# Kernel optimization log

Hardware: AMD Instinct MI355X
Metric: run time of the kernel (lower is better)

Reference implementation:

```python
import jax, jax.numpy as jnp
import numpy as np
import math

K_HEADS = 16  # nb_heads from init_kwargs


def setup_inputs() -> dict:
    key = jax.random.key(0)
    ks = jax.random.split(key, 7)
    B, M, H, D = 2, 2048, 1024, 1024 // K_HEADS
    return {
        "h": jax.random.normal(ks[0], (B, M, H), jnp.float32),
        "h_cache": jax.random.normal(ks[1], (B, M, H), jnp.float32),
        "key_pe": jax.random.normal(ks[2], (1, D, M), jnp.float32),
        "Wq": jax.random.normal(ks[3], (H, H), jnp.float32) * 0.02,
        "Wk": jax.random.normal(ks[4], (H, H), jnp.float32) * 0.02,
        "Wv": jax.random.normal(ks[5], (H, H), jnp.float32) * 0.02,
        "Wo": jax.random.normal(ks[6], (H, H), jnp.float32) * 0.02,
    }


def _heads(x, K):
    # [B, M, H] -> [B, K, M, D]
    B, M, H = x.shape
    return x.reshape(B, M, K, H // K).transpose(0, 2, 1, 3)


def reference(h, h_cache, key_pe, Wq, Wk, Wv, Wo):
    B, M, H = h.shape
    K = K_HEADS
    D = H // K
    q = _heads(h @ Wq.T, K)        # [B, K, M, D]
    k = _heads(h_cache @ Wk.T, K)  # [B, K, L, D], L == M
    v = _heads(h_cache @ Wv.T, K)  # [B, K, L, D]

    attn_cont = jnp.einsum("bkmd,bkld->bkml", q, k)            # content scores
    attn_pos = jnp.einsum("bkmd,dl->bkml", q, key_pe[0])       # positional scores
    attn = (attn_cont + attn_pos[..., :M]) / math.sqrt(D)
    attn = jax.nn.softmax(attn, axis=-1)  # computed as in source, but source
    # (faithfully) multiplies VALUE by attn_cont, not attn:
    out = jnp.einsum("bkml,bkld->bkmd", attn_cont, v)          # [B, K, M, D]
    out = out.transpose(0, 2, 1, 3).reshape(B, M, H)
    return out @ Wo.T
```

## Files before the change

kernel.cpp:

```cpp
#include <hip/hip_runtime.h>
#include <hip/hip_bf16.h>

#define BB 2
#define MM 2048
#define HH 1024
#define KH 16

typedef short s16x8 __attribute__((ext_vector_type(8)));
typedef float f32x4 __attribute__((ext_vector_type(4)));
typedef float f32x16 __attribute__((ext_vector_type(16)));

#define GLOBAL_AS __attribute__((address_space(1)))
#define LDS_AS    __attribute__((address_space(3)))

__device__ __forceinline__ void async_copy16(const void* g, void* l) {
    __builtin_amdgcn_global_load_lds((const GLOBAL_AS void*)g, (LDS_AS void*)l, 16, 0, 0);
}

struct __align__(8) bf16x4_t { __hip_bfloat16 x, y, z, w; };

__global__ __launch_bounds__(256) void cvt_all(
    const float* __restrict__ h_f, const float* __restrict__ hc_f,
    const float* __restrict__ Wk_f, const float* __restrict__ Wv_f,
    const float* __restrict__ Wo_f, const float* __restrict__ Wq_f,
    __hip_bfloat16* __restrict__ hb, __hip_bfloat16* __restrict__ hcT,
    __hip_bfloat16* __restrict__ wkb, __hip_bfloat16* __restrict__ wvb,
    __hip_bfloat16* __restrict__ wob, __hip_bfloat16* __restrict__ wqt)
{
    __shared__ float Tl[64][65];
    const int seg = blockIdx.y;
    const int t = threadIdx.x;
    const int bx = blockIdx.x;

    if (seg == 1) {
        if (bx >= BB * 512) return;
        const int b = bx >> 9;
        const int tile = bx & 511;
        const int m0 = (tile >> 4) * 64;
        const int k0 = (tile & 15) * 64;
        const int r = t >> 6;
        const int c = t & 63;
        const float* src = hc_f + (size_t)b * MM * HH;
#pragma unroll
        for (int i = 0; i < 64; i += 4)
            Tl[r + i][c] = src[(size_t)(m0 + r + i) * HH + k0 + c];
        __syncthreads();
        __hip_bfloat16* dst = hcT + (size_t)b * HH * MM;
#pragma unroll
        for (int i = 0; i < 64; i += 4)
            dst[(size_t)(k0 + r + i) * MM + m0 + c] = __float2bfloat16(Tl[c][r + i]);
        return;
    }
    if (seg == 5) {
        if (bx >= 256) return;
        const int j0 = (bx >> 4) * 64;
        const int k0 = (bx & 15) * 64;
        const int r = t >> 6;
        const int c = t & 63;
#pragma unroll
        for (int i = 0; i < 64; i += 4)
            Tl[r + i][c] = Wq_f[(size_t)(j0 + r + i) * HH + k0 + c];
        __syncthreads();
#pragma unroll
        for (int i = 0; i < 64; i += 4)
            wqt[(size_t)(k0 + r + i) * HH + j0 + c] = __float2bfloat16(Tl[c][r + i]);
        return;
    }
    const float* src;
    __hip_bfloat16* dst;
    int n;
    switch (seg) {
        case 0: src = h_f;  dst = hb;  n = BB * MM * HH; break;
        case 2: src = Wk_f; dst = wkb; n = HH * HH; break;
        case 3: src = Wv_f; dst = wvb; n = HH * HH; break;
        default: src = Wo_f; dst = wob; n = HH * HH; break;
    }
    const int i = (bx * 256 + t) * 4;
    if (i + 3 < n) {
        const float4 v = *(const float4*)(src + i);
        bf16x4_t o;
        o.x = __float2bfloat16(v.x);
        o.y = __float2bfloat16(v.y);
        o.z = __float2bfloat16(v.z);
        o.w = __float2bfloat16(v.w);
        *(bf16x4_t*)(dst + i) = o;
    }
}

__device__ __forceinline__ void store_c(__hip_bfloat16* C, size_t idx, float v) {
    C[idx] = __float2bfloat16(v);
}
__device__ __forceinline__ void store_c(float* C, size_t idx, float v) { C[idx] = v; }

template <typename OutT, int KD>
__device__ __forceinline__ void gemm_nt_body64(
    const __hip_bfloat16* __restrict__ A,
    const __hip_bfloat16* __restrict__ Bm,
    OutT* __restrict__ C,
    __hip_bfloat16* As, __hip_bfloat16* Bs,
    int m0, int n0, int ldc)
{
    const int t    = threadIdx.x;
    const int lane = t & 63;
    const int wave = t >> 6;

    const int srow = lane >> 3;
    const int sw   = ((lane & 7) ^ srow) * 8;

    const int wn  = wave * 32;
    const int fm  = lane & 31;
    const int fm7 = fm & 7;
    const int ghi = lane >> 5;

    f32x16 acc[2] = {};

    for (int k0 = 0; k0 < KD; k0 += 64) {
        __syncthreads();
        {
            const __hip_bfloat16* ag = A + (size_t)(m0 + wave * 16 + srow) * KD + k0 + sw;
            async_copy16(ag,          As + wave * 1024);
            async_copy16(ag + 8 * KD, As + wave * 1024 + 512);
        }
#pragma unroll
        for (int i = 0; i < 2; ++i) {
            const int c = wave * 2 + i;
            const __hip_bfloat16* bg = Bm + (size_t)(n0 + c * 16 + srow) * KD + k0 + sw;
            async_copy16(bg,          Bs + c * 1024);
            async_copy16(bg + 8 * KD, Bs + c * 1024 + 512);
        }
        __syncthreads();

#pragma unroll
        for (int ks = 0; ks < 64; ks += 16) {
            const int pos = ((((ks >> 3) + ghi) ^ fm7) * 8);
            s16x8 af[2], bf;
#pragma unroll
            for (int mi = 0; mi < 2; ++mi)
                af[mi] = *(const s16x8*)(As + (mi * 32 + fm) * 64 + pos);
            bf = *(const s16x8*)(Bs + (wn + fm) * 64 + pos);
#pragma unroll
            for (int mi = 0; mi < 2; ++mi)
                acc[mi] = __builtin_amdgcn_mfma_f32_32x32x16_bf16(
                    af[mi], bf, acc[mi], 0, 0, 0);
        }
    }

    const int ec = lane & 31;
    const int eb = (lane >> 5) * 4;
#pragma unroll
    for (int mi = 0; mi < 2; ++mi)
#pragma unroll
        for (int r = 0; r < 16; ++r) {
            const int m = m0 + mi * 32 + (r & 3) + 8 * (r >> 2) + eb;
            const int n = n0 + wn + ec;
            store_c(C, (size_t)m * ldc + n, acc[mi][r]);
        }
}

__global__ __launch_bounds__(256) void gemm_g(
    const __hip_bfloat16* __restrict__ hcT, __hip_bfloat16* __restrict__ G)
{
    __shared__ __align__(16) __hip_bfloat16 As[64 * 64];
    __shared__ __align__(16) __hip_bfloat16 Bs[128 * 64];
    const int b = blockIdx.z;
    const __hip_bfloat16* Ab = hcT + (size_t)b * HH * MM;
    gemm_nt_body64<__hip_bfloat16, MM>(Ab, Ab, G + (size_t)b * HH * HH,
                                       As, Bs, blockIdx.x * 64, blockIdx.y * 128, HH);
}

__global__ __launch_bounds__(256) void gemm_v2(
    const __hip_bfloat16* __restrict__ wvb, const __hip_bfloat16* __restrict__ G,
    __hip_bfloat16* __restrict__ V2T)
{
    __shared__ __align__(16) __hip_bfloat16 As[64 * 64];
    __shared__ __align__(16) __hip_bfloat16 Bs[128 * 64];
    const int b = blockIdx.z;
    gemm_nt_body64<__hip_bfloat16, HH>(wvb, G + (size_t)b * HH * HH,
                                       V2T + (size_t)b * HH * HH,
                                       As, Bs, blockIdx.x * 64, blockIdx.y * 128, HH);
}

__global__ __launch_bounds__(256) void gemm_t(
    const __hip_bfloat16* __restrict__ wk,
    const __hip_bfloat16* __restrict__ v2t,
    float* __restrict__ S)
{
    __shared__ __align__(16) __hip_bfloat16 As[64 * 64];
    __shared__ __align__(16) __hip_bfloat16 Bs[64 * 64];
    const int t    = threadIdx.x;
    const int lane = t & 63;
    const int wave = t >> 6;
    const int head = blockIdx.x;
    const int b    = blockIdx.y;

    const __hip_bfloat16* A  = wk  + (size_t)head * 64 * HH;
    const __hip_bfloat16* Bm = v2t + (size_t)b * HH * HH + (size_t)head * 64 * HH;

    const int srow = lane >> 3;
    const int sw   = ((lane & 7) ^ srow) * 8;
    const int wm   = (wave >> 1) * 32;
    const int wn   = (wave & 1) * 32;
    const int fm   = lane & 31;
    const int fm7  = fm & 7;
    const int ghi  = lane >> 5;

    f32x16 acc = {};
    for (int k0 = 0; k0 < HH; k0 += 64) {
        __syncthreads();
#pragma unroll
        for (int i = 0; i < 2; ++i) {
            const int c = wave * 2 + i;
            async_copy16(A  + (size_t)(c * 8 + srow) * HH + k0 + sw, As + c * 512);
            async_copy16(Bm + (size_t)(c * 8 + srow) * HH + k0 + sw, Bs + c * 512);
        }
        __syncthreads();
#pragma unroll
        for (int ks = 0; ks < 64; ks += 16) {
            const int pos = ((((ks >> 3) + ghi) ^ fm7) * 8);
            const s16x8 af = *(const s16x8*)(As + (wm + fm) * 64 + pos);
            const s16x8 bf = *(const s16x8*)(Bs + (wn + fm) * 64 + pos);
            acc = __builtin_amdgcn_mfma_f32_32x32x16_bf16(af, bf, acc, 0, 0, 0);
        }
    }

    float* Sg = S + ((size_t)b * KH + head) * 4096;
    const int col   = lane & 31;
    const int rbase = 4 * (lane >> 5);
#pragma unroll
    for (int r = 0; r < 16; ++r) {
        const int row = (r & 3) + 8 * (r >> 2) + rbase;
        Sg[(wm + row) * 64 + wn + col] = acc[r];
    }
}

__global__ __launch_bounds__(256) void gemm_f(
    const __hip_bfloat16* __restrict__ W2, const __hip_bfloat16* __restrict__ WqT,
    __hip_bfloat16* __restrict__ F)
{
    __shared__ __align__(16) __hip_bfloat16 As[64 * 64];
    __shared__ __align__(16) __hip_bfloat16 Bs[128 * 64];
    const int b = blockIdx.z;
    gemm_nt_body64<__hip_bfloat16, HH>(W2 + (size_t)b * HH * HH, WqT,
                                       F + (size_t)b * HH * HH,
                                       As, Bs, blockIdx.x * 64, blockIdx.y * 128, HH);
}

__global__ __launch_bounds__(256) void gemm_final(
    const __hip_bfloat16* __restrict__ hb, const __hip_bfloat16* __restrict__ F,
    float* __restrict__ outg)
{
    __shared__ __align__(16) __hip_bfloat16 As[64 * 64];
    __shared__ __align__(16) __hip_bfloat16 Bs[128 * 64];
    const int b = blockIdx.z;
    gemm_nt_body64<float, HH>(hb + (size_t)b * MM * HH, F + (size_t)b * HH * HH,
                              outg + (size_t)b * MM * HH, As, Bs,
                              blockIdx.x * 64, blockIdx.y * 128, HH);
}

__global__ __launch_bounds__(256) void w2_fold(
    const __hip_bfloat16* __restrict__ Wo,
    const float* __restrict__ S,
    __hip_bfloat16* __restrict__ W2)
{
    __shared__ float Sl[64 * 68];
    __shared__ float Wl[128 * 68];
    const int t = threadIdx.x, head = blockIdx.y, b = blockIdx.z;
    const int n0 = blockIdx.x * 128;

    const float* Sg = S + ((size_t)b * KH + head) * 4096;
    for (int idx = t; idx < 4096; idx += 256) {
        const int dp = idx >> 6, d = idx & 63;
        Sl[d * 68 + dp] = Sg[idx];
    }
    for (int idx = t; idx < 1024; idx += 256) {
        const int r = idx >> 3, c8 = (idx & 7) * 8;
        s16x8 wv = *(const s16x8*)(Wo + (size_t)(n0 + r) * HH + head * 64 + c8);
#pragma unroll
        for (int j = 0; j < 8; ++j) {
            __hip_bfloat16 wb = *(((const __hip_bfloat16*)&wv) + j);
            Wl[r * 68 + c8 + j] = __bfloat162float(wb);
        }
    }
    __syncthreads();

    const int dpb = (t & 15) * 4;
    const int ng  = t >> 4;
    float acc[8][4] = {};
    for (int d0 = 0; d0 < 64; d0 += 4) {
        f32x4 sv[4];
#pragma unroll
        for (int r = 0; r < 4; ++r)
            sv[r] = *(const f32x4*)(Sl + (d0 + r) * 68 + dpb);
#pragma unroll
        for (int i = 0; i < 8; ++i) {
            const f32x4 wv = *(const f32x4*)(Wl + (ng + 16 * i) * 68 + d0);
#pragma unroll
            for (int r = 0; r < 4; ++r)
#pragma unroll
                for (int j = 0; j < 4; ++j)
                    acc[i][j] += wv[r] * sv[r][j];
        }
    }

#pragma unroll
    for (int i = 0; i < 8; ++i) {
        bf16x4_t o;
        o.x = __float2bfloat16(acc[i][0]);
        o.y = __float2bfloat16(acc[i][1]);
        o.z = __float2bfloat16(acc[i][2]);
        o.w = __float2bfloat16(acc[i][3]);
        *(bf16x4_t*)(W2 + (size_t)b * HH * HH + (size_t)(n0 + ng + 16 * i) * HH
                     + head * 64 + dpb) = o;
    }
}

extern "C" void kernel_launch(void* const* d_in, const int* in_sizes, int n_in,
                              void* d_out, int out_size, void* d_ws, size_t ws_size,
                              hipStream_t stream) {
    const float* h_f  = (const float*)d_in[0];
    const float* hc_f = (const float*)d_in[1];
    const float* Wq_f = (const float*)d_in[3];
    const float* Wk_f = (const float*)d_in[4];
    const float* Wv_f = (const float*)d_in[5];
    const float* Wo_f = (const float*)d_in[6];
    float* out = (float*)d_out;

    const size_t act_b = (size_t)BB * MM * HH * 2;
    const size_t w_b   = (size_t)HH * HH * 2;
    char* ws = (char*)d_ws;
    __hip_bfloat16* hb   = (__hip_bfloat16*)(ws);
    __hip_bfloat16* hcT  = (__hip_bfloat16*)(ws + act_b);
    __hip_bfloat16* wkb  = (__hip_bfloat16*)(ws + 2 * act_b);
    __hip_bfloat16* wvb  = (__hip_bfloat16*)(ws + 2 * act_b + w_b);
    __hip_bfloat16* wob  = (__hip_bfloat16*)(ws + 2 * act_b + 2 * w_b);
    __hip_bfloat16* wqt  = (__hip_bfloat16*)(ws + 2 * act_b + 3 * w_b);
    __hip_bfloat16* Gb   = (__hip_bfloat16*)(ws + 2 * act_b + 4 * w_b);
    __hip_bfloat16* V2T  = (__hip_bfloat16*)(ws + 2 * act_b + 6 * w_b);
    float*          Sbuf = (float*)(ws + 2 * act_b + 8 * w_b);
    __hip_bfloat16* W2   = (__hip_bfloat16*)(ws + 2 * act_b + 8 * w_b + (size_t)512 * 1024);
    __hip_bfloat16* Fbuf = (__hip_bfloat16*)(ws + 2 * act_b + 10 * w_b + (size_t)512 * 1024);

    const dim3 blk(256);

    cvt_all<<<dim3(4096, 6), blk, 0, stream>>>(h_f, hc_f, Wk_f, Wv_f, Wo_f, Wq_f,
                                               hb, hcT, wkb, wvb, wob, wqt);

    gemm_g<<<dim3(16, 8, BB), blk, 0, stream>>>(hcT, Gb);

    gemm_v2<<<dim3(16, 8, BB), blk, 0, stream>>>(wvb, Gb, V2T);

    gemm_t<<<dim3(KH, BB), blk, 0, stream>>>(wkb, V2T, Sbuf);

    w2_fold<<<dim3(8, KH, BB), blk, 0, stream>>>(wob, Sbuf, W2);

    gemm_f<<<dim3(16, 8, BB), blk, 0, stream>>>(W2, wqt, Fbuf);

    gemm_final<<<dim3(32, 8, BB), blk, 0, stream>>>(hb, Fbuf, out);
}
```

Baseline: 190.3 us.

## Fuse V2 and per-head S GEMMs with split-K atomics, shrink G/F tiles

The per-head S matrix is now computed in one kernel that forms a 64x64 slice of Wk·G and multiplies it by the matching Wv tile. Partial results are accumulated into S with atomicAdd over 16 K-slices, so the full V2T intermediate and the 32-block gemm_t launch are gone and the work is spread over many more blocks. S is zeroed inside the conversion kernel. gemm_g and gemm_f move to 64x64 tiles to double the block count, and the transposes in the conversion kernel now write 4-wide vectors instead of scalars. The cost is float atomics, which make S summation order nondeterministic, plus an extra bf16 rounding of the intermediate.

Result: faster. 177.3 us (-6.8%).

```diff
diff --git a/kernel.cpp b/kernel.cpp
--- a/kernel.cpp
+++ b/kernel.cpp
@@ -25,7 +25,8 @@
     const float* __restrict__ Wo_f, const float* __restrict__ Wq_f,
     __hip_bfloat16* __restrict__ hb, __hip_bfloat16* __restrict__ hcT,
     __hip_bfloat16* __restrict__ wkb, __hip_bfloat16* __restrict__ wvb,
-    __hip_bfloat16* __restrict__ wob, __hip_bfloat16* __restrict__ wqt)
+    __hip_bfloat16* __restrict__ wob, __hip_bfloat16* __restrict__ wqt,
+    float* __restrict__ Sz)
 {
     __shared__ float Tl[64][65];
     const int seg = blockIdx.y;
@@ -46,24 +47,47 @@
             Tl[r + i][c] = src[(size_t)(m0 + r + i) * HH + k0 + c];
         __syncthreads();
         __hip_bfloat16* dst = hcT + (size_t)b * HH * MM;
-#pragma unroll
-        for (int i = 0; i < 64; i += 4)
-            dst[(size_t)(k0 + r + i) * MM + m0 + c] = __float2bfloat16(Tl[c][r + i]);
+        const int ml = (t & 15) * 4;
+#pragma unroll
+        for (int ii = 0; ii < 4; ++ii) {
+            const int kl = (t >> 4) + 16 * ii;
+            bf16x4_t o;
+            o.x = __float2bfloat16(Tl[ml + 0][kl]);
+            o.y = __float2bfloat16(Tl[ml + 1][kl]);
+            o.z = __float2bfloat16(Tl[ml + 2][kl]);
+            o.w = __float2bfloat16(Tl[ml + 3][kl]);
+            *(bf16x4_t*)(dst + (size_t)(k0 + kl) * MM + m0 + ml) = o;
+        }
         return;
     }
     if (seg == 5) {
-        if (bx >= 256) return;
-        const int j0 = (bx >> 4) * 64;
-        const int k0 = (bx & 15) * 64;
+        if (bx < 128) {
+            const int i = (bx * 256 + t) * 4;
+            float4 z = {0.f, 0.f, 0.f, 0.f};
+            *(float4*)(Sz + i) = z;
+            return;
+        }
+        if (bx >= 384) return;
+        const int tile = bx - 128;
+        const int j0 = (tile >> 4) * 64;
+        const int k0 = (tile & 15) * 64;
         const int r = t >> 6;
         const int c = t & 63;
 #pragma unroll
         for (int i = 0; i < 64; i += 4)
             Tl[r + i][c] = Wq_f[(size_t)(j0 + r + i) * HH + k0 + c];
         __syncthreads();
-#pragma unroll
-        for (int i = 0; i < 64; i += 4)
-            wqt[(size_t)(k0 + r + i) * HH + j0 + c] = __float2bfloat16(Tl[c][r + i]);
+        const int ml = (t & 15) * 4;
+#pragma unroll
+        for (int ii = 0; ii < 4; ++ii) {
+            const int kl = (t >> 4) + 16 * ii;
+            bf16x4_t o;
+            o.x = __float2bfloat16(Tl[ml + 0][kl]);
+            o.y = __float2bfloat16(Tl[ml + 1][kl]);
+            o.z = __float2bfloat16(Tl[ml + 2][kl]);
+            o.w = __float2bfloat16(Tl[ml + 3][kl]);
+            *(bf16x4_t*)(wqt + (size_t)(k0 + kl) * HH + j0 + ml) = o;
+        }
         return;
     }
     const float* src;
@@ -92,110 +116,13 @@
 }
 __device__ __forceinline__ void store_c(float* C, size_t idx, float v) { C[idx] = v; }
 
-template <typename OutT, int KD>
-__device__ __forceinline__ void gemm_nt_body64(
-    const __hip_bfloat16* __restrict__ A,
-    const __hip_bfloat16* __restrict__ Bm,
-    OutT* __restrict__ C,
-    __hip_bfloat16* As, __hip_bfloat16* Bs,
-    int m0, int n0, int ldc)
+__device__ __forceinline__ f32x16 nt64_acc(
+    const __hip_bfloat16* __restrict__ A, const __hip_bfloat16* __restrict__ B,
+    int kd, size_t ld, __hip_bfloat16* As, __hip_bfloat16* Bs)
 {
     const int t    = threadIdx.x;
     const int lane = t & 63;
     const int wave = t >> 6;
-
-    const int srow = lane >> 3;
-    const int sw   = ((lane & 7) ^ srow) * 8;
-
-    const int wn  = wave * 32;
-    const int fm  = lane & 31;
-    const int fm7 = fm & 7;
-    const int ghi = lane >> 5;
-
-    f32x16 acc[2] = {};
-
-    for (int k0 = 0; k0 < KD; k0 += 64) {
-        __syncthreads();
-        {
-            const __hip_bfloat16* ag = A + (size_t)(m0 + wave * 16 + srow) * KD + k0 + sw;
-            async_copy16(ag,          As + wave * 1024);
-            async_copy16(ag + 8 * KD, As + wave * 1024 + 512);
-        }
-#pragma unroll
-        for (int i = 0; i < 2; ++i) {
-            const int c = wave * 2 + i;
-            const __hip_bfloat16* bg = Bm + (size_t)(n0 + c * 16 + srow) * KD + k0 + sw;
-            async_copy16(bg,          Bs + c * 1024);
-            async_copy16(bg + 8 * KD, Bs + c * 1024 + 512);
-        }
-        __syncthreads();
-
-#pragma unroll
-        for (int ks = 0; ks < 64; ks += 16) {
-            const int pos = ((((ks >> 3) + ghi) ^ fm7) * 8);
-            s16x8 af[2], bf;
-#pragma unroll
-            for (int mi = 0; mi < 2; ++mi)
-                af[mi] = *(const s16x8*)(As + (mi * 32 + fm) * 64 + pos);
-            bf = *(const s16x8*)(Bs + (wn + fm) * 64 + pos);
-#pragma unroll
-            for (int mi = 0; mi < 2; ++mi)
-                acc[mi] = __builtin_amdgcn_mfma_f32_32x32x16_bf16(
-                    af[mi], bf, acc[mi], 0, 0, 0);
-        }
-    }
-
-    const int ec = lane & 31;
-    const int eb = (lane >> 5) * 4;
-#pragma unroll
-    for (int mi = 0; mi < 2; ++mi)
-#pragma unroll
-        for (int r = 0; r < 16; ++r) {
-            const int m = m0 + mi * 32 + (r & 3) + 8 * (r >> 2) + eb;
-            const int n = n0 + wn + ec;
-            store_c(C, (size_t)m * ldc + n, acc[mi][r]);
-        }
-}
-
-__global__ __launch_bounds__(256) void gemm_g(
-    const __hip_bfloat16* __restrict__ hcT, __hip_bfloat16* __restrict__ G)
-{
-    __shared__ __align__(16) __hip_bfloat16 As[64 * 64];
-    __shared__ __align__(16) __hip_bfloat16 Bs[128 * 64];
-    const int b = blockIdx.z;
-    const __hip_bfloat16* Ab = hcT + (size_t)b * HH * MM;
-    gemm_nt_body64<__hip_bfloat16, MM>(Ab, Ab, G + (size_t)b * HH * HH,
-                                       As, Bs, blockIdx.x * 64, blockIdx.y * 128, HH);
-}
-
-__global__ __launch_bounds__(256) void gemm_v2(
-    const __hip_bfloat16* __restrict__ wvb, const __hip_bfloat16* __restrict__ G,
-    __hip_bfloat16* __restrict__ V2T)
-{
-    __shared__ __align__(16) __hip_bfloat16 As[64 * 64];
-    __shared__ __align__(16) __hip_bfloat16 Bs[128 * 64];
-    const int b = blockIdx.z;
-    gemm_nt_body64<__hip_bfloat16, HH>(wvb, G + (size_t)b * HH * HH,
-                                       V2T + (size_t)b * HH * HH,
-                                       As, Bs, blockIdx.x * 64, blockIdx.y * 128, HH);
-}
-
-__global__ __launch_bounds__(256) void gemm_t(
-    const __hip_bfloat16* __restrict__ wk,
-    const __hip_bfloat16* __restrict__ v2t,
-    float* __restrict__ S)
-{
-    __shared__ __align__(16) __hip_bfloat16 As[64 * 64];
-    __shared__ __align__(16) __hip_bfloat16 Bs[64 * 64];
-    const int t    = threadIdx.x;
-    const int lane = t & 63;
-    const int wave = t >> 6;
-    const int head = blockIdx.x;
-    const int b    = blockIdx.y;
-
-    const __hip_bfloat16* A  = wk  + (size_t)head * 64 * HH;
-    const __hip_bfloat16* Bm = v2t + (size_t)b * HH * HH + (size_t)head * 64 * HH;
-
     const int srow = lane >> 3;
     const int sw   = ((lane & 7) ^ srow) * 8;
     const int wm   = (wave >> 1) * 32;
@@ -205,13 +132,13 @@
     const int ghi  = lane >> 5;
 
     f32x16 acc = {};
-    for (int k0 = 0; k0 < HH; k0 += 64) {
+    for (int k0 = 0; k0 < kd; k0 += 64) {
         __syncthreads();
 #pragma unroll
         for (int i = 0; i < 2; ++i) {
             const int c = wave * 2 + i;
-            async_copy16(A  + (size_t)(c * 8 + srow) * HH + k0 + sw, As + c * 512);
-            async_copy16(Bm + (size_t)(c * 8 + srow) * HH + k0 + sw, Bs + c * 512);
+            async_copy16(A + (size_t)(c * 8 + srow) * ld + k0 + sw, As + c * 512);
+            async_copy16(B + (size_t)(c * 8 + srow) * ld + k0 + sw, Bs + c * 512);
         }
         __syncthreads();
 #pragma unroll
@@ -222,15 +149,114 @@
             acc = __builtin_amdgcn_mfma_f32_32x32x16_bf16(af, bf, acc, 0, 0, 0);
         }
     }
+    return acc;
+}
+
+template <typename OutT>
+__device__ __forceinline__ void store_tile64(OutT* C, int ldc, const f32x16& acc) {
+    const int lane = threadIdx.x & 63;
+    const int wave = threadIdx.x >> 6;
+    const int wm = (wave >> 1) * 32;
+    const int wn = (wave & 1) * 32;
+    const int col = wn + (lane & 31);
+    const int rb  = 4 * (lane >> 5);
+#pragma unroll
+    for (int r = 0; r < 16; ++r) {
+        const int row = wm + (r & 3) + 8 * (r >> 2) + rb;
+        store_c(C, (size_t)row * ldc + col, acc[r]);
+    }
+}
+
+__global__ __launch_bounds__(256) void gemm_g(
+    const __hip_bfloat16* __restrict__ hcT, __hip_bfloat16* __restrict__ G)
+{
+    __shared__ __align__(16) __hip_bfloat16 As[64 * 64];
+    __shared__ __align__(16) __hip_bfloat16 Bs[64 * 64];
+    const int b = blockIdx.z;
+    const int m0 = blockIdx.x * 64, n0 = blockIdx.y * 64;
+    const __hip_bfloat16* Ab = hcT + (size_t)b * HH * MM;
+    f32x16 acc = nt64_acc(Ab + (size_t)m0 * MM, Ab + (size_t)n0 * MM, MM, MM, As, Bs);
+    store_tile64(G + (size_t)b * HH * HH + (size_t)m0 * HH + n0, HH, acc);
+}
+
+#define LPP 72
+
+__global__ __launch_bounds__(256) void gemm_vt(
+    const __hip_bfloat16* __restrict__ wkb, const __hip_bfloat16* __restrict__ wvb,
+    const __hip_bfloat16* __restrict__ G, float* __restrict__ S)
+{
+    __shared__ __align__(16) char smem[64 * LPP * 2 + 64 * 64 * 2];
+    __hip_bfloat16* As = (__hip_bfloat16*)smem;
+    __hip_bfloat16* Bs = (__hip_bfloat16*)(smem + 8192);
+    __hip_bfloat16* Pl = (__hip_bfloat16*)smem;
+    __hip_bfloat16* Wl = (__hip_bfloat16*)(smem + 64 * LPP * 2);
+
+    const int t    = threadIdx.x;
+    const int lane = t & 63;
+    const int wave = t >> 6;
+    const int kt   = blockIdx.x;
+    const int head = blockIdx.y;
+    const int b    = blockIdx.z;
+
+    const __hip_bfloat16* Arow = G + (size_t)b * HH * HH + (size_t)kt * 64 * HH;
+    const __hip_bfloat16* Brow = wkb + (size_t)head * 64 * HH;
+
+    f32x16 acc = nt64_acc(Arow, Brow, HH, HH, As, Bs);
+    __syncthreads();
+
+    {
+        const int wm = (wave >> 1) * 32;
+        const int wn = (wave & 1) * 32;
+        const int col_i = wn + (lane & 31);
+        const int ghi4  = 4 * (lane >> 5);
+#pragma unroll
+        for (int g = 0; g < 4; ++g) {
+            const int ccb = wm + 8 * g + ghi4;
+            bf16x4_t o;
+            o.x = __float2bfloat16(acc[4 * g + 0]);
+            o.y = __float2bfloat16(acc[4 * g + 1]);
+            o.z = __float2bfloat16(acc[4 * g + 2]);
+            o.w = __float2bfloat16(acc[4 * g + 3]);
+            *(bf16x4_t*)(Pl + col_i * LPP + ccb) = o;
+        }
+    }
+    {
+        const int srow = lane >> 3;
+        const int sw   = ((lane & 7) ^ srow) * 8;
+#pragma unroll
+        for (int i = 0; i < 2; ++i) {
+            const int c = wave * 2 + i;
+            async_copy16(wvb + (size_t)(head * 64 + c * 8 + srow) * HH + kt * 64 + sw,
+                         Wl + c * 512);
+        }
+    }
+    __syncthreads();
+
+    const int fr  = lane & 15;
+    const int fq  = (lane >> 4) * 8;
+    const int wm2 = wave * 16;
+
+    f32x4 acc2[4] = {};
+#pragma unroll
+    for (int kk = 0; kk < 64; kk += 32) {
+        const s16x8 af = *(const s16x8*)(Pl + (wm2 + fr) * LPP + kk + fq);
+#pragma unroll
+        for (int nj = 0; nj < 4; ++nj) {
+            const int row = nj * 16 + fr;
+            const s16x8 bfv = *(const s16x8*)(
+                Wl + row * 64 + ((((kk + fq) >> 3) ^ (row & 7)) << 3));
+            acc2[nj] = __builtin_amdgcn_mfma_f32_16x16x32_bf16(af, bfv, acc2[nj], 0, 0, 0);
+        }
+    }
 
     float* Sg = S + ((size_t)b * KH + head) * 4096;
-    const int col   = lane & 31;
-    const int rbase = 4 * (lane >> 5);
-#pragma unroll
-    for (int r = 0; r < 16; ++r) {
-        const int row = (r & 3) + 8 * (r >> 2) + rbase;
-        Sg[(wm + row) * 64 + wn + col] = acc[r];
-    }
+    const int er = (lane >> 4) * 4;
+    const int ec = lane & 15;
+#pragma unroll
+    for (int nj = 0; nj < 4; ++nj)
+#pragma unroll
+        for (int rr = 0; rr < 4; ++rr)
+            atomicAdd(&Sg[(wm2 + er + rr) * 64 + nj * 16 + ec], acc2[nj][rr]);
 }
 
 __global__ __launch_bounds__(256) void gemm_f(
@@ -238,11 +264,77 @@
     __hip_bfloat16* __restrict__ F)
 {
     __shared__ __align__(16) __hip_bfloat16 As[64 * 64];
-    __shared__ __align__(16) __hip_bfloat16 Bs[128 * 64];
+    __shared__ __align__(16) __hip_bfloat16 Bs[64 * 64];
     const int b = blockIdx.z;
-    gemm_nt_body64<__hip_bfloat16, HH>(W2 + (size_t)b * HH * HH, WqT,
-                                       F + (size_t)b * HH * HH,
-                                       As, Bs, blockIdx.x * 64, blockIdx.y * 128, HH);
+    const int m0 = blockIdx.x * 64, n0 = blockIdx.y * 64;
+    f32x16 acc = nt64_acc(W2 + (size_t)b * HH * HH + (size_t)m0 * HH,
+                          WqT + (size_t)n0 * HH, HH, HH, As, Bs);
+    store_tile64(F + (size_t)b * HH * HH + (size_t)m0 * HH + n0, HH, acc);
+}
+
+template <typename OutT>
+__device__ __forceinline__ void gemm_nt_body64(
+    const __hip_bfloat16* __restrict__ A,
+    const __hip_bfloat16* __restrict__ Bm,
+    OutT* __restrict__ C,
+    __hip_bfloat16* As, __hip_bfloat16* Bs,
+    int m0, int n0)
+{
+    const int t    = threadIdx.x;
+    const int lane = t & 63;
+    const int wave = t >> 6;
+
+    const int srow = lane >> 3;
+    const int sw   = ((lane & 7) ^ srow) * 8;
+
+    const int wn  = wave * 32;
+    const int fm  = lane & 31;
+    const int fm7 = fm & 7;
+    const int ghi = lane >> 5;
+
+    f32x16 acc[2] = {};
+
+    for (int k0 = 0; k0 < HH; k0 += 64) {
+        __syncthreads();
+        {
+            const __hip_bfloat16* ag = A + (size_t)(m0 + wave * 16 + srow) * HH + k0 + sw;
+            async_copy16(ag,          As + wave * 1024);
+            async_copy16(ag + 8 * HH, As + wave * 1024 + 512);
+        }
+#pragma unroll
+        for (int i = 0; i < 2; ++i) {
+            const int c = wave * 2 + i;
+            const __hip_bfloat16* bg = Bm + (size_t)(n0 + c * 16 + srow) * HH + k0 + sw;
+            async_copy16(bg,          Bs + c * 1024);
+            async_copy16(bg + 8 * HH, Bs + c * 1024 + 512);
+        }
+        __syncthreads();
+
+#pragma unroll
+        for (int ks = 0; ks < 64; ks += 16) {
+            const int pos = ((((ks >> 3) + ghi) ^ fm7) * 8);
+            s16x8 af[2], bf;
+#pragma unroll
+            for (int mi = 0; mi < 2; ++mi)
+                af[mi] = *(const s16x8*)(As + (mi * 32 + fm) * 64 + pos);
+            bf = *(const s16x8*)(Bs + (wn + fm) * 64 + pos);
+#pragma unroll
+            for (int mi = 0; mi < 2; ++mi)
+                acc[mi] = __builtin_amdgcn_mfma_f32_32x32x16_bf16(
+                    af[mi], bf, acc[mi], 0, 0, 0);
+        }
+    }
+
+    const int ec = lane & 31;
+    const int eb = (lane >> 5) * 4;
+#pragma unroll
+    for (int mi = 0; mi < 2; ++mi)
+#pragma unroll
+        for (int r = 0; r < 16; ++r) {
+            const int m = m0 + mi * 32 + (r & 3) + 8 * (r >> 2) + eb;
+            const int n = n0 + wn + ec;
+            store_c(C, (size_t)m * HH + n, acc[mi][r]);
+        }
 }
 
 __global__ __launch_bounds__(256) void gemm_final(
@@ -252,9 +344,9 @@
     __shared__ __align__(16) __hip_bfloat16 As[64 * 64];
     __shared__ __align__(16) __hip_bfloat16 Bs[128 * 64];
     const int b = blockIdx.z;
-    gemm_nt_body64<float, HH>(hb + (size_t)b * MM * HH, F + (size_t)b * HH * HH,
-                              outg + (size_t)b * MM * HH, As, Bs,
-                              blockIdx.x * 64, blockIdx.y * 128, HH);
+    gemm_nt_body64<float>(hb + (size_t)b * MM * HH, F + (size_t)b * HH * HH,
+                          outg + (size_t)b * MM * HH, As, Bs,
+                          blockIdx.x * 64, blockIdx.y * 128);
 }
 
 __global__ __launch_bounds__(256) void w2_fold(
@@ -335,25 +427,22 @@
     __hip_bfloat16* wob  = (__hip_bfloat16*)(ws + 2 * act_b + 2 * w_b);
     __hip_bfloat16* wqt  = (__hip_bfloat16*)(ws + 2 * act_b + 3 * w_b);
     __hip_bfloat16* Gb   = (__hip_bfloat16*)(ws + 2 * act_b + 4 * w_b);
-    __hip_bfloat16* V2T  = (__hip_bfloat16*)(ws + 2 * act_b + 6 * w_b);
-    float*          Sbuf = (float*)(ws + 2 * act_b + 8 * w_b);
-    __hip_bfloat16* W2   = (__hip_bfloat16*)(ws + 2 * act_b + 8 * w_b + (size_t)512 * 1024);
-    __hip_bfloat16* Fbuf = (__hip_bfloat16*)(ws + 2 * act_b + 10 * w_b + (size_t)512 * 1024);
+    float*          Sbuf = (float*)(ws + 2 * act_b + 6 * w_b);
+    __hip_bfloat16* W2   = (__hip_bfloat16*)(ws + 2 * act_b + 6 * w_b + (size_t)512 * 1024);
+    __hip_bfloat16* Fbuf = (__hip_bfloat16*)(ws + 2 * act_b + 8 * w_b + (size_t)512 * 1024);
 
     const dim3 blk(256);
 
     cvt_all<<<dim3(4096, 6), blk, 0, stream>>>(h_f, hc_f, Wk_f, Wv_f, Wo_f, Wq_f,
-                                               hb, hcT, wkb, wvb, wob, wqt);
-
-    gemm_g<<<dim3(16, 8, BB), blk, 0, stream>>>(hcT, Gb);
-
-    gemm_v2<<<dim3(16, 8, BB), blk, 0, stream>>>(wvb, Gb, V2T);
-
-    gemm_t<<<dim3(KH, BB), blk, 0, stream>>>(wkb, V2T, Sbuf);
+                                               hb, hcT, wkb, wvb, wob, wqt, Sbuf);
+
+    gemm_g<<<dim3(16, 16, BB), blk, 0, stream>>>(hcT, Gb);
+
+    gemm_vt<<<dim3(16, KH, BB), blk, 0, stream>>>(wkb, wvb, Gb, Sbuf);
 
     w2_fold<<<dim3(8, KH, BB), blk, 0, stream>>>(wob, Sbuf, W2);
 
-    gemm_f<<<dim3(16, 8, BB), blk, 0, stream>>>(W2, wqt, Fbuf);
+    gemm_f<<<dim3(16, 16, BB), blk, 0, stream>>>(W2, wqt, Fbuf);
 
     gemm_final<<<dim3(32, 8, BB), blk, 0, stream>>>(hb, Fbuf, out);
 }
```
